# Optimization experiments

Measured on AMD Instinct MI355X. Metric: run time of the kernel, lower is better.

The kernel has to match this reference:

```python
import jax, jax.numpy as jnp
import numpy as np

N, K, D = 32768, 4096, 256


def setup_inputs() -> dict:
    key = jax.random.key(0)
    k1, k2 = jax.random.split(key)
    z_e = jax.random.normal(k1, (N, D), dtype=jnp.float32)
    embed = jax.random.normal(k2, (K, D), dtype=jnp.float32)
    return {"z_e": z_e, "embed": embed}


def reference(z_e, embed):
    # squared L2 distances: ||z||^2 - 2 z.E^T + ||e||^2  -> [N, K]
    d = (jnp.sum(z_e * z_e, axis=1, keepdims=True)
         - 2.0 * (z_e @ embed.T)
         + jnp.sum(embed * embed, axis=1))
    idx = jnp.argmin(d, axis=1)                      # [N] int32
    one_hot = jax.nn.one_hot(idx, K, dtype=z_e.dtype)  # [N, K]
    z_q = one_hot @ embed                            # [N, D] (matches torch's one_hot @ embed)
    return (z_q, idx, one_hot)
```

## Files before the change

### kernel.cpp

```cpp
#include <hip/hip_runtime.h>


#define N_TOK 32768
#define K_CODE 4096
#define D_DIM 256
#define BM 64

typedef float f32x4 __attribute__((ext_vector_type(4)));
typedef short s16x8 __attribute__((ext_vector_type(8)));
typedef int   i32x4 __attribute__((ext_vector_type(4)));

#define OUT_FLOATS 142639104u
#define SCR_FLOATS 1576960u
#define SCR_OFF    (OUT_FLOATS - SCR_FLOATS)
#define EFRAG_SHORTS (3u * K_CODE * D_DIM)

static __device__ __forceinline__ unsigned short f2bf(float f) {
    unsigned int u = __float_as_uint(f);
    u = (u + 0x7fffu + ((u >> 16) & 1u)) >> 16;
    return (unsigned short)u;
}
static __device__ __forceinline__ float bf2f(unsigned short b) {
    return __uint_as_float(((unsigned int)b) << 16);
}

__global__ __launch_bounds__(256) void vq_prep(const float* __restrict__ embed,
                                               float* __restrict__ out) {
    __shared__ float part[8][33];
    unsigned short* escr = (unsigned short*)(out + SCR_OFF);
    float* e2g = out + SCR_OFF + (EFRAG_SHORTS / 2);

    const int t    = threadIdx.x;
    const int cl   = t >> 5;
    const int r32  = t & 31;
    const int dc   = r32 >> 2;
    const int quad = r32 & 3;
    const int k    = blockIdx.x * 8 + cl;

    const float* src = embed + (size_t)k * D_DIM + dc * 32 + quad * 8;
    float x[8];
    *(float4*)(x)     = *(const float4*)(src);
    *(float4*)(x + 4) = *(const float4*)(src + 4);

    s16x8 hv, mv, lv;
    float s2 = 0.0f;
#pragma unroll
    for (int j = 0; j < 8; ++j) {
        const float xx = x[j];
        s2 += xx * xx;
        const unsigned short bh = f2bf(xx);
        const float r1 = xx - bf2f(bh);
        const unsigned short bm = f2bf(r1);
        const float r2 = r1 - bf2f(bm);
        hv[j] = (short)bh; mv[j] = (short)bm; lv[j] = (short)f2bf(r2);
    }

    const int ct_g = k >> 4;
    const int lane = quad * 16 + (k & 15);
    const size_t base = ((size_t)(ct_g * 8 + dc) * 3) * 512 + lane * 8;
    *(s16x8*)&escr[base]        = hv;
    *(s16x8*)&escr[base + 512]  = mv;
    *(s16x8*)&escr[base + 1024] = lv;

    part[cl][r32] = s2;
    __syncthreads();
    if (t < 8) {
        float s = 0.0f;
#pragma unroll
        for (int j = 0; j < 32; ++j) s += part[t][j];
        e2g[blockIdx.x * 8 + t] = s;
    }
}

__global__ __launch_bounds__(512, 2)
void vq_argmin_mfma(const float* __restrict__ z_e, float* __restrict__ out) {
    __shared__ __align__(16) short As[49152];
    __shared__ float redv[64][9];
    __shared__ int   redi[64][9];

    const unsigned short* escr = (const unsigned short*)(out + SCR_OFF);
    const float* e2g = out + SCR_OFF + (EFRAG_SHORTS / 2);

    const int t    = threadIdx.x;
    const int w    = t >> 6;
    const int lane = t & 63;
    const int n    = lane & 15;
    const int quad = lane >> 4;
    const int row0 = blockIdx.x * BM;

#pragma unroll
    for (int i = 0; i < 4; ++i) {
        const int run  = t + 512 * i;
        const int qs   = run & 3;
        const int dcs  = (run >> 2) & 7;
        const int row  = run >> 5;
        const float* src = z_e + (size_t)(row0 + row) * D_DIM + dcs * 32 + qs * 8;
        float x[8];
        *(float4*)(x)     = *(const float4*)(src);
        *(float4*)(x + 4) = *(const float4*)(src + 4);
        s16x8 hv, mv, lv;
#pragma unroll
        for (int j = 0; j < 8; ++j) {
            const float xx = x[j];
            const unsigned short bh = f2bf(xx);
            const float r1 = xx - bf2f(bh);
            const unsigned short bm = f2bf(r1);
            hv[j] = (short)bh; mv[j] = (short)bm; lv[j] = (short)f2bf(r1 - bf2f(bm));
        }
        const int rtile = row >> 4;
        const int ls    = qs * 16 + (row & 15);
        *(s16x8*)&As[((0 * 4 + rtile) * 8 + dcs) * 512 + ls * 8] = hv;
        *(s16x8*)&As[((1 * 4 + rtile) * 8 + dcs) * 512 + ls * 8] = mv;
        *(s16x8*)&As[((2 * 4 + rtile) * 8 + dcs) * 512 + ls * 8] = lv;
    }
    __syncthreads();

    float bv[16];
    int   bidx[16];
#pragma unroll
    for (int s = 0; s < 16; ++s) { bv[s] = 3.0e38f; bidx[s] = 0; }

#pragma unroll 1
    for (int kt = 0; kt < 16; ++kt) {
        f32x4 acc[4][2];
#pragma unroll
        for (int rt = 0; rt < 4; ++rt)
#pragma unroll
            for (int u = 0; u < 2; ++u) acc[rt][u] = (f32x4){0.f, 0.f, 0.f, 0.f};

#pragma unroll 1
        for (int dc = 0; dc < 8; ++dc) {
            s16x8 bfm[2][3];
#pragma unroll
            for (int u = 0; u < 2; ++u) {
                const int ct_g = kt * 16 + w * 2 + u;
#pragma unroll
                for (int c = 0; c < 3; ++c)
                    bfm[u][c] = *(const s16x8*)&escr[((size_t)(ct_g * 8 + dc) * 3 + c) * 512 + lane * 8];
            }
#pragma unroll
            for (int rt = 0; rt < 4; ++rt) {
                s16x8 af0 = *(const s16x8*)&As[((0 * 4 + rt) * 8 + dc) * 512 + lane * 8];
                s16x8 af1 = *(const s16x8*)&As[((1 * 4 + rt) * 8 + dc) * 512 + lane * 8];
                s16x8 af2 = *(const s16x8*)&As[((2 * 4 + rt) * 8 + dc) * 512 + lane * 8];
#pragma unroll
                for (int u = 0; u < 2; ++u) {
                    f32x4 a = acc[rt][u];
                    a = __builtin_amdgcn_mfma_f32_16x16x32_bf16(af0, bfm[u][0], a, 0, 0, 0);
                    a = __builtin_amdgcn_mfma_f32_16x16x32_bf16(af0, bfm[u][1], a, 0, 0, 0);
                    a = __builtin_amdgcn_mfma_f32_16x16x32_bf16(af1, bfm[u][0], a, 0, 0, 0);
                    a = __builtin_amdgcn_mfma_f32_16x16x32_bf16(af1, bfm[u][1], a, 0, 0, 0);
                    a = __builtin_amdgcn_mfma_f32_16x16x32_bf16(af0, bfm[u][2], a, 0, 0, 0);
                    a = __builtin_amdgcn_mfma_f32_16x16x32_bf16(af2, bfm[u][0], a, 0, 0, 0);
                    acc[rt][u] = a;
                }
            }
        }

#pragma unroll
        for (int u = 0; u < 2; ++u) {
            const int  code = kt * 256 + (w * 2 + u) * 16 + n;
            const float e2v = e2g[code];
#pragma unroll
            for (int rt = 0; rt < 4; ++rt)
#pragma unroll
                for (int r = 0; r < 4; ++r) {
                    const float val = fmaf(-2.0f, acc[rt][u][r], e2v);
                    const int slot = rt * 4 + r;
                    if (val < bv[slot]) { bv[slot] = val; bidx[slot] = code; }
                }
        }
    }

#pragma unroll
    for (int slot = 0; slot < 16; ++slot) {
#pragma unroll
        for (int mask = 1; mask < 16; mask <<= 1) {
            const float ov = __shfl_xor(bv[slot], mask);
            const int   oi = __shfl_xor(bidx[slot], mask);
            if (ov < bv[slot] || (ov == bv[slot] && oi < bidx[slot])) {
                bv[slot] = ov; bidx[slot] = oi;
            }
        }
    }
    if (n == 0) {
#pragma unroll
        for (int rt = 0; rt < 4; ++rt)
#pragma unroll
            for (int r = 0; r < 4; ++r) {
                const int row_local = rt * 16 + quad * 4 + r;
                redv[row_local][w] = bv[rt * 4 + r];
                redi[row_local][w] = bidx[rt * 4 + r];
            }
    }
    __syncthreads();
    if (t < 64) {
        float v = redv[t][0];
        int  bi = redi[t][0];
#pragma unroll
        for (int j = 1; j < 8; ++j) {
            const float v2 = redv[t][j];
            const int   i2 = redi[t][j];
            if (v2 < v || (v2 == v && i2 < bi)) { v = v2; bi = i2; }
        }
        out[(size_t)N_TOK * D_DIM + (size_t)(row0 + t)] = (float)bi;
    }
}

__launch_bounds__(256, 8)
__global__ void vq_epilogue(const float* __restrict__ embed,
                            float* __restrict__ out) {
    __shared__ int bks[16];
    const int t    = threadIdx.x;
    const int w    = t >> 6;
    const int lane = t & 63;
    const int row0 = blockIdx.x * 16;

    const float* idxf = out + (size_t)N_TOK * D_DIM;
    float* zq = out;
    float* oh = out + (size_t)N_TOK * D_DIM + N_TOK;

    if (t < 16) bks[t] = (int)idxf[row0 + t];
    __syncthreads();

#pragma unroll 1
    for (int rr = 0; rr < 4; ++rr) {
        const int r   = rr * 4 + w;
        const int row = row0 + r;
        const int bk  = bks[r];

        f32x4 v = *(const f32x4*)&embed[(size_t)bk * D_DIM + lane * 4];
        __builtin_nontemporal_store(v, (f32x4*)&zq[(size_t)row * D_DIM + lane * 4]);

        float* ohrow = &oh[(size_t)row * K_CODE];
#pragma unroll
        for (int g = 0; g < 16; ++g) {
            const int base = (g * 64 + lane) * 4;
            f32x4 u;
            u.x = (bk == base    ) ? 1.0f : 0.0f;
            u.y = (bk == base + 1) ? 1.0f : 0.0f;
            u.z = (bk == base + 2) ? 1.0f : 0.0f;
            u.w = (bk == base + 3) ? 1.0f : 0.0f;
            __builtin_nontemporal_store(u, (f32x4*)&ohrow[base]);
        }
    }
}

extern "C" void kernel_launch(void* const* d_in, const int* in_sizes, int n_in,
                              void* d_out, int out_size, void* d_ws, size_t ws_size,
                              hipStream_t stream) {
    const float* z_e   = (const float*)d_in[0];
    const float* embed = (const float*)d_in[1];
    float* out = (float*)d_out;

    hipLaunchKernelGGL(vq_prep,        dim3(K_CODE / 8), dim3(256), 0, stream, embed, out);
    hipLaunchKernelGGL(vq_argmin_mfma, dim3(N_TOK / BM), dim3(512), 0, stream, z_e, out);
    hipLaunchKernelGGL(vq_epilogue,    dim3(N_TOK / 16), dim3(256), 0, stream, embed, out);
}
```

Before: 874.1 us.

## Fuse one-hot/z_q epilogue into argmin kernel and double-buffer codebook fragments

Flattens the kt/dc loops into a single software-pipelined loop that prefetches the next step's B fragments from global memory into a second register buffer while the current step's MFMAs run. The z_q gather and most of the one-hot writes move into the argmin kernel, so each block writes its own rows right after computing indices. Rows at or above OH_SAFE_ROWS are handled by a small tail kernel, because the scratch codebook region lives at the end of the output buffer and must not be overwritten while other blocks still read it. The cost is higher register pressure and a longer per-block tail, which may affect occupancy.

```diff
diff --git a/kernel.cpp b/kernel.cpp
--- a/kernel.cpp
+++ b/kernel.cpp
@@ -8,12 +8,12 @@
 
 typedef float f32x4 __attribute__((ext_vector_type(4)));
 typedef short s16x8 __attribute__((ext_vector_type(8)));
-typedef int   i32x4 __attribute__((ext_vector_type(4)));
 
 #define OUT_FLOATS 142639104u
 #define SCR_FLOATS 1576960u
 #define SCR_OFF    (OUT_FLOATS - SCR_FLOATS)
 #define EFRAG_SHORTS (3u * K_CODE * D_DIM)
+#define OH_SAFE_ROWS 32320
 
 static __device__ __forceinline__ unsigned short f2bf(float f) {
     unsigned int u = __float_as_uint(f);
@@ -51,8 +51,7 @@
         const unsigned short bh = f2bf(xx);
         const float r1 = xx - bf2f(bh);
         const unsigned short bm = f2bf(r1);
-        const float r2 = r1 - bf2f(bm);
-        hv[j] = (short)bh; mv[j] = (short)bm; lv[j] = (short)f2bf(r2);
+        hv[j] = (short)bh; mv[j] = (short)bm; lv[j] = (short)f2bf(r1 - bf2f(bm));
     }
 
     const int ct_g = k >> 4;
@@ -72,11 +71,72 @@
     }
 }
 
+static __device__ __forceinline__ void load_b(const unsigned short* __restrict__ escr,
+                                              int kt, int dc, int w, int lane,
+                                              s16x8 (&buf)[2][3]) {
+#pragma unroll
+    for (int u = 0; u < 2; ++u) {
+        const int ct_g = kt * 16 + w * 2 + u;
+        const unsigned short* p = &escr[((size_t)(ct_g * 8 + dc) * 3) * 512 + lane * 8];
+#pragma unroll
+        for (int c = 0; c < 3; ++c)
+            buf[u][c] = *(const s16x8*)(p + c * 512);
+    }
+}
+
+static __device__ __forceinline__ void proc_step(const short* As,
+        const float* __restrict__ e2g, int kt, int dc, int w, int lane, int n,
+        s16x8 (&bfm)[2][3], f32x4 (&acc)[4][2], float (&e2r)[2],
+        float (&bv)[16], int (&bidx)[16]) {
+    if (dc == 0) {
+#pragma unroll
+        for (int u = 0; u < 2; ++u) e2r[u] = e2g[kt * 256 + (w * 2 + u) * 16 + n];
+    }
+#pragma unroll
+    for (int rt = 0; rt < 4; ++rt) {
+        s16x8 af0 = *(const s16x8*)&As[((0 * 4 + rt) * 8 + dc) * 512 + lane * 8];
+        s16x8 af1 = *(const s16x8*)&As[((1 * 4 + rt) * 8 + dc) * 512 + lane * 8];
+        s16x8 af2 = *(const s16x8*)&As[((2 * 4 + rt) * 8 + dc) * 512 + lane * 8];
+#pragma unroll
+        for (int u = 0; u < 2; ++u) {
+            f32x4 a = acc[rt][u];
+            a = __builtin_amdgcn_mfma_f32_16x16x32_bf16(af0, bfm[u][0], a, 0, 0, 0);
+            a = __builtin_amdgcn_mfma_f32_16x16x32_bf16(af0, bfm[u][1], a, 0, 0, 0);
+            a = __builtin_amdgcn_mfma_f32_16x16x32_bf16(af1, bfm[u][0], a, 0, 0, 0);
+            a = __builtin_amdgcn_mfma_f32_16x16x32_bf16(af1, bfm[u][1], a, 0, 0, 0);
+            a = __builtin_amdgcn_mfma_f32_16x16x32_bf16(af0, bfm[u][2], a, 0, 0, 0);
+            a = __builtin_amdgcn_mfma_f32_16x16x32_bf16(af2, bfm[u][0], a, 0, 0, 0);
+            acc[rt][u] = a;
+        }
+    }
+    if (dc == 7) {
+#pragma unroll
+        for (int u = 0; u < 2; ++u) {
+            const int code = kt * 256 + (w * 2 + u) * 16 + n;
+#pragma unroll
+            for (int rt = 0; rt < 4; ++rt)
+#pragma unroll
+                for (int r = 0; r < 4; ++r) {
+                    const float val = fmaf(-2.0f, acc[rt][u][r], e2r[u]);
+                    const int slot = rt * 4 + r;
+                    if (val < bv[slot]) { bv[slot] = val; bidx[slot] = code; }
+                }
+        }
+#pragma unroll
+        for (int rt = 0; rt < 4; ++rt)
+#pragma unroll
+            for (int u = 0; u < 2; ++u) acc[rt][u] = (f32x4){0.f, 0.f, 0.f, 0.f};
+    }
+}
+
 __global__ __launch_bounds__(512, 2)
-void vq_argmin_mfma(const float* __restrict__ z_e, float* __restrict__ out) {
+void vq_argmin_mfma(const float* __restrict__ z_e,
+                    const float* __restrict__ embed,
+                    float* __restrict__ out) {
     __shared__ __align__(16) short As[49152];
     __shared__ float redv[64][9];
     __shared__ int   redi[64][9];
+    __shared__ int   bk_lds[64];
 
     const unsigned short* escr = (const unsigned short*)(out + SCR_OFF);
     const float* e2g = out + SCR_OFF + (EFRAG_SHORTS / 2);
@@ -120,56 +180,23 @@
 #pragma unroll
     for (int s = 0; s < 16; ++s) { bv[s] = 3.0e38f; bidx[s] = 0; }
 
+    f32x4 acc[4][2];
+#pragma unroll
+    for (int rt = 0; rt < 4; ++rt)
+#pragma unroll
+        for (int u = 0; u < 2; ++u) acc[rt][u] = (f32x4){0.f, 0.f, 0.f, 0.f};
+
+    float e2r[2];
+    s16x8 b0[2][3], b1[2][3];
+    load_b(escr, 0, 0, w, lane, b0);
+
 #pragma unroll 1
-    for (int kt = 0; kt < 16; ++kt) {
-        f32x4 acc[4][2];
-#pragma unroll
-        for (int rt = 0; rt < 4; ++rt)
-#pragma unroll
-            for (int u = 0; u < 2; ++u) acc[rt][u] = (f32x4){0.f, 0.f, 0.f, 0.f};
-
-#pragma unroll 1
-        for (int dc = 0; dc < 8; ++dc) {
-            s16x8 bfm[2][3];
-#pragma unroll
-            for (int u = 0; u < 2; ++u) {
-                const int ct_g = kt * 16 + w * 2 + u;
-#pragma unroll
-                for (int c = 0; c < 3; ++c)
-                    bfm[u][c] = *(const s16x8*)&escr[((size_t)(ct_g * 8 + dc) * 3 + c) * 512 + lane * 8];
-            }
-#pragma unroll
-            for (int rt = 0; rt < 4; ++rt) {
-                s16x8 af0 = *(const s16x8*)&As[((0 * 4 + rt) * 8 + dc) * 512 + lane * 8];
-                s16x8 af1 = *(const s16x8*)&As[((1 * 4 + rt) * 8 + dc) * 512 + lane * 8];
-                s16x8 af2 = *(const s16x8*)&As[((2 * 4 + rt) * 8 + dc) * 512 + lane * 8];
-#pragma unroll
-                for (int u = 0; u < 2; ++u) {
-                    f32x4 a = acc[rt][u];
-                    a = __builtin_amdgcn_mfma_f32_16x16x32_bf16(af0, bfm[u][0], a, 0, 0, 0);
-                    a = __builtin_amdgcn_mfma_f32_16x16x32_bf16(af0, bfm[u][1], a, 0, 0, 0);
-                    a = __builtin_amdgcn_mfma_f32_16x16x32_bf16(af1, bfm[u][0], a, 0, 0, 0);
-                    a = __builtin_amdgcn_mfma_f32_16x16x32_bf16(af1, bfm[u][1], a, 0, 0, 0);
-                    a = __builtin_amdgcn_mfma_f32_16x16x32_bf16(af0, bfm[u][2], a, 0, 0, 0);
-                    a = __builtin_amdgcn_mfma_f32_16x16x32_bf16(af2, bfm[u][0], a, 0, 0, 0);
-                    acc[rt][u] = a;
-                }
-            }
-        }
-
-#pragma unroll
-        for (int u = 0; u < 2; ++u) {
-            const int  code = kt * 256 + (w * 2 + u) * 16 + n;
-            const float e2v = e2g[code];
-#pragma unroll
-            for (int rt = 0; rt < 4; ++rt)
-#pragma unroll
-                for (int r = 0; r < 4; ++r) {
-                    const float val = fmaf(-2.0f, acc[rt][u][r], e2v);
-                    const int slot = rt * 4 + r;
-                    if (val < bv[slot]) { bv[slot] = val; bidx[slot] = code; }
-                }
-        }
+    for (int it = 0; it < 64; ++it) {
+        const int s0 = it * 2, s1 = s0 + 1, s2 = s1 + 1;
+        load_b(escr, s1 >> 3, s1 & 7, w, lane, b1);
+        proc_step(As, e2g, s0 >> 3, s0 & 7, w, lane, n, b0, acc, e2r, bv, bidx);
+        if (it < 63) load_b(escr, s2 >> 3, s2 & 7, w, lane, b0);
+        proc_step(As, e2g, s1 >> 3, s1 & 7, w, lane, n, b1, acc, e2r, bv, bidx);
     }
 
 #pragma unroll
@@ -203,21 +230,52 @@
             const int   i2 = redi[t][j];
             if (v2 < v || (v2 == v && i2 < bi)) { v = v2; bi = i2; }
         }
+        bk_lds[t] = bi;
         out[(size_t)N_TOK * D_DIM + (size_t)(row0 + t)] = (float)bi;
     }
+    __syncthreads();
+
+    float* zq = out;
+    float* oh = out + (size_t)N_TOK * D_DIM + N_TOK;
+
+#pragma unroll 1
+    for (int rr = 0; rr < 8; ++rr) {
+        const int rl  = w * 8 + rr;
+        const int row = row0 + rl;
+        const int bk  = bk_lds[rl];
+        f32x4 v = *(const f32x4*)&embed[(size_t)bk * D_DIM + lane * 4];
+        __builtin_nontemporal_store(v, (f32x4*)&zq[(size_t)row * D_DIM + lane * 4]);
+    }
+    if (row0 < OH_SAFE_ROWS) {
+#pragma unroll 1
+        for (int rr = 0; rr < 8; ++rr) {
+            const int rl  = w * 8 + rr;
+            const int row = row0 + rl;
+            const int bk  = bk_lds[rl];
+            float* ohrow = &oh[(size_t)row * K_CODE];
+#pragma unroll
+            for (int g = 0; g < 16; ++g) {
+                const int base = (g * 64 + lane) * 4;
+                f32x4 u;
+                u.x = (bk == base    ) ? 1.0f : 0.0f;
+                u.y = (bk == base + 1) ? 1.0f : 0.0f;
+                u.z = (bk == base + 2) ? 1.0f : 0.0f;
+                u.w = (bk == base + 3) ? 1.0f : 0.0f;
+                __builtin_nontemporal_store(u, (f32x4*)&ohrow[base]);
+            }
+        }
+    }
 }
 
 __launch_bounds__(256, 8)
-__global__ void vq_epilogue(const float* __restrict__ embed,
-                            float* __restrict__ out) {
+__global__ void vq_oh_tail(float* __restrict__ out) {
     __shared__ int bks[16];
     const int t    = threadIdx.x;
     const int w    = t >> 6;
     const int lane = t & 63;
-    const int row0 = blockIdx.x * 16;
+    const int row0 = OH_SAFE_ROWS + blockIdx.x * 16;
 
     const float* idxf = out + (size_t)N_TOK * D_DIM;
-    float* zq = out;
     float* oh = out + (size_t)N_TOK * D_DIM + N_TOK;
 
     if (t < 16) bks[t] = (int)idxf[row0 + t];
@@ -228,10 +286,6 @@
         const int r   = rr * 4 + w;
         const int row = row0 + r;
         const int bk  = bks[r];
-
-        f32x4 v = *(const f32x4*)&embed[(size_t)bk * D_DIM + lane * 4];
-        __builtin_nontemporal_store(v, (f32x4*)&zq[(size_t)row * D_DIM + lane * 4]);
-
         float* ohrow = &oh[(size_t)row * K_CODE];
 #pragma unroll
         for (int g = 0; g < 16; ++g) {
@@ -254,6 +308,6 @@
     float* out = (float*)d_out;
 
     hipLaunchKernelGGL(vq_prep,        dim3(K_CODE / 8), dim3(256), 0, stream, embed, out);
-    hipLaunchKernelGGL(vq_argmin_mfma, dim3(N_TOK / BM), dim3(512), 0, stream, z_e, out);
-    hipLaunchKernelGGL(vq_epilogue,    dim3(N_TOK / 16), dim3(256), 0, stream, embed, out);
-}
+    hipLaunchKernelGGL(vq_argmin_mfma, dim3(N_TOK / BM), dim3(512), 0, stream, z_e, embed, out);
+    hipLaunchKernelGGL(vq_oh_tail,     dim3((N_TOK - OH_SAFE_ROWS) / 16), dim3(256), 0, stream, out);
+}
```

Result: faster. 853.9 us (-2.3%).
